# Optimization experiments

Hardware: AMD Instinct MI355X
Metric: run time of the kernel (lower is better)

## Reference

```python
import jax, jax.numpy as jnp
import numpy as np

NUM_HEADS = 8
NUM_POINTS = 4


def _grid_sample_bilinear(img, grid, H, W):
    """torch F.grid_sample(mode='bilinear', padding='zeros', align_corners=False).
    img:  [B, H, W, D]   grid: [B, S, 2] with (x, y) in [-1, 1].
    Returns [B, S, D].
    """
    gx, gy = grid[..., 0], grid[..., 1]
    # align_corners=False pixel mapping
    x = ((gx + 1.0) * W - 1.0) * 0.5
    y = ((gy + 1.0) * H - 1.0) * 0.5
    x0 = jnp.floor(x)
    y0 = jnp.floor(y)
    wx1 = x - x0
    wy1 = y - y0
    x0i = x0.astype(jnp.int32)
    y0i = y0.astype(jnp.int32)
    img_flat = img.reshape(img.shape[0], H * W, img.shape[-1])  # [B, N, D]

    def corner(xi, yi, w):
        valid = (xi >= 0) & (xi < W) & (yi >= 0) & (yi < H)  # zeros padding
        idx = jnp.clip(yi, 0, H - 1) * W + jnp.clip(xi, 0, W - 1)  # [B, S]
        v = jnp.take_along_axis(img_flat, idx[..., None], axis=1)  # [B, S, D]
        return v * (w * valid.astype(img.dtype))[..., None]

    out = corner(x0i, y0i, (1.0 - wx1) * (1.0 - wy1))
    out += corner(x0i + 1, y0i, wx1 * (1.0 - wy1))
    out += corner(x0i, y0i + 1, (1.0 - wx1) * wy1)
    out += corner(x0i + 1, y0i + 1, wx1 * wy1)
    return out


def setup_inputs() -> dict:
    key = jax.random.key(0)
    ks = jax.random.split(key, 12)
    B, Q, D = 4, 1024, 256
    H, W = 128, 128
    nh, npts = NUM_HEADS, NUM_POINTS
    f32 = jnp.float32
    return {
        "query": jax.random.normal(ks[0], (B, Q, D), f32),
        "reference_points": jax.random.uniform(ks[1], (B, Q, 2), f32),
        "value": jax.random.normal(ks[2], (B, H * W, D), f32),
        "W_off": jax.random.normal(ks[3], (D, nh * npts * 2), f32) * 0.02,
        "b_off": jax.random.normal(ks[4], (nh * npts * 2,), f32) * 0.02,
        "W_attn": jax.random.normal(ks[5], (D, nh * npts), f32) * 0.02,
        "b_attn": jax.random.normal(ks[6], (nh * npts,), f32) * 0.02,
        "W_v": jax.random.normal(ks[7], (D, D), f32) * (D ** -0.5),
        "b_v": jnp.zeros((D,), f32),
        "W_out": jax.random.normal(ks[8], (nh * D, D), f32) * ((nh * D) ** -0.5),
        "b_out": jnp.zeros((D,), f32),
        "H": H,
        "W": W,
    }


def reference(query, reference_points, value, W_off, b_off, W_attn, b_attn,
              W_v, b_v, W_out, b_out, H, W):
    B, Q, D = query.shape
    nh, npts = NUM_HEADS, NUM_POINTS
    # learned offsets and per-point attention weights
    offsets = (query @ W_off + b_off).reshape(B, Q, nh, npts, 2)
    attn = jax.nn.softmax((query @ W_attn + b_attn).reshape(B, Q, nh, npts), axis=-1)
    # sampling locations in [-1, 1]
    locs = reference_points[:, :, None, None, :] + offsets * 0.1
    locs = jnp.clip(locs, 0.0, 1.0) * 2.0 - 1.0
    # value projection -> 2D feature map [B, H, W, D]
    img = (value @ W_v + b_v).reshape(B, H, W, D)
    # sample all heads/points at once
    grid = locs.reshape(B, Q * nh * npts, 2)
    sampled = _grid_sample_bilinear(img, grid, H, W).reshape(B, Q, nh, npts, D)
    # weighted reduce over points, concat heads
    weighted = jnp.einsum("bqhpd,bqhp->bqhd", sampled, attn)
    out = weighted.reshape(B, Q, nh * D) @ W_out + b_out
    return out
```

## Files before the change

kernel.cpp:

```cpp
#include <hip/hip_runtime.h>
#include <hip/hip_bf16.h>
#include <math.h>

constexpr int B  = 4;
constexpr int Q  = 1024;
constexpr int D  = 256;
constexpr int NH = 8;
constexpr int NP = 4;
constexpr int H  = 128;
constexpr int W  = 128;
constexpr int HW = H * W;
constexpr int KAUG = 2112;

typedef short   bf16x8  __attribute__((ext_vector_type(8)));
typedef float   f32x4   __attribute__((ext_vector_type(4)));
typedef short   short4v __attribute__((ext_vector_type(4)));
typedef unsigned short ushort8v __attribute__((ext_vector_type(8)));

__device__ inline unsigned short f2bf(float f) {
    union { float f; unsigned u; } v; v.f = f;
    unsigned r = v.u + 0x7fff + ((v.u >> 16) & 1);
    return (unsigned short)(r >> 16);
}
__device__ inline float bf2f(unsigned short s) {
    union { unsigned u; float f; } v; v.u = ((unsigned)s) << 16;
    return v.f;
}

__device__ inline void async16(const void* g, void* l) {
    __builtin_amdgcn_global_load_lds(
        (const __attribute__((address_space(1))) unsigned*)g,
        (__attribute__((address_space(3))) unsigned*)l, 16, 0, 0);
}

__device__ __forceinline__ void gemm64_dbuf(
        unsigned short* __restrict__ lds,
        const unsigned short* __restrict__ A, int lda,
        const unsigned short* __restrict__ Bt, int ldb,
        const float* __restrict__ bias,
        float* __restrict__ C, int ldc, int K, int m0, int n0) {
    const int tid  = threadIdx.x;
    const int lane = tid & 63;
    const int w    = tid >> 6;
    const int wm   = w >> 1, wn = w & 1;

    const int srow = w * 8 + (lane >> 3);
    const int schk = (lane & 7) ^ (lane >> 3);
    const unsigned short* ag0 = A  + (size_t)(m0 + srow)      * lda + schk * 8;
    const unsigned short* ag1 = A  + (size_t)(m0 + srow + 32) * lda + schk * 8;
    const unsigned short* bg0 = Bt + (size_t)(n0 + srow)      * ldb + schk * 8;
    const unsigned short* bg1 = Bt + (size_t)(n0 + srow + 32) * ldb + schk * 8;
    const int l0 = w * 512 + lane * 8;
    const int l1 = l0 + 2048;

    int aoff[2][2], boff[2][2];
    #pragma unroll
    for (int i = 0; i < 2; ++i)
        #pragma unroll
        for (int kk = 0; kk < 2; ++kk) {
            const int ar = wm * 32 + i * 16 + (lane & 15);
            aoff[i][kk] = ar * 64 + ((((lane >> 4) + kk * 4) ^ (ar & 7)) * 8);
            const int br = wn * 32 + i * 16 + (lane & 15);
            boff[i][kk] = br * 64 + ((((lane >> 4) + kk * 4) ^ (br & 7)) * 8);
        }

    f32x4 acc[2][2];
    #pragma unroll
    for (int i = 0; i < 2; ++i)
        #pragma unroll
        for (int j = 0; j < 2; ++j) acc[i][j] = (f32x4){0.f, 0.f, 0.f, 0.f};

    async16(ag0, &lds[0 * 4096 + l0]); async16(ag1, &lds[0 * 4096 + l1]);
    async16(bg0, &lds[1 * 4096 + l0]); async16(bg1, &lds[1 * 4096 + l1]);

    const int niter = K >> 6;
    for (int it = 0; it < niter; ++it) {
        __syncthreads();
        const int cur = (it & 1) * 2;
        if (it + 1 < niter) {
            const int nxt = 2 - cur;
            const int ko  = (it + 1) * 64;
            async16(ag0 + ko, &lds[nxt * 4096 + l0]);
            async16(ag1 + ko, &lds[nxt * 4096 + l1]);
            async16(bg0 + ko, &lds[(nxt + 1) * 4096 + l0]);
            async16(bg1 + ko, &lds[(nxt + 1) * 4096 + l1]);
        }
        bf16x8 af[2][2], bfv[2][2];
        #pragma unroll
        for (int i = 0; i < 2; ++i)
            #pragma unroll
            for (int kk = 0; kk < 2; ++kk) {
                af[i][kk]  = *(const bf16x8*)&lds[cur * 4096 + aoff[i][kk]];
                bfv[i][kk] = *(const bf16x8*)&lds[(cur + 1) * 4096 + boff[i][kk]];
            }
        #pragma unroll
        for (int i = 0; i < 2; ++i)
            #pragma unroll
            for (int j = 0; j < 2; ++j)
                #pragma unroll
                for (int kk = 0; kk < 2; ++kk)
                    acc[i][j] = __builtin_amdgcn_mfma_f32_16x16x32_bf16(
                        af[i][kk], bfv[j][kk], acc[i][j], 0, 0, 0);
    }

    const int colb = n0 + wn * 32 + (lane & 15);
    const int rowb = m0 + wm * 32 + (lane >> 4) * 4;
    #pragma unroll
    for (int j = 0; j < 2; ++j) {
        const int col = colb + j * 16;
        const float bb = bias[col];
        #pragma unroll
        for (int i = 0; i < 2; ++i)
            #pragma unroll
            for (int r = 0; r < 4; ++r)
                C[(size_t)(rowb + i * 16 + r) * ldc + col] = acc[i][j][r] + bb;
    }
}

__device__ __forceinline__ void gemm64_single_t(
        unsigned short* __restrict__ lds,
        const unsigned short* __restrict__ A, int lda,
        const unsigned short* __restrict__ Bt, int ldb,
        unsigned short* __restrict__ Wt, int ldc, int K,
        int m0, int n0, int zblk) {
    const int tid  = threadIdx.x;
    const int lane = tid & 63;
    const int w    = tid >> 6;
    const int wm   = w >> 1, wn = w & 1;
    Bt += (size_t)zblk * 256;

    const int srow = w * 8 + (lane >> 3);
    const int schk = (lane & 7) ^ (lane >> 3);
    const unsigned short* ag0 = A  + (size_t)(m0 + srow)      * lda + schk * 8;
    const unsigned short* ag1 = A  + (size_t)(m0 + srow + 32) * lda + schk * 8;
    const unsigned short* bg0 = Bt + (size_t)(n0 + srow)      * ldb + schk * 8;
    const unsigned short* bg1 = Bt + (size_t)(n0 + srow + 32) * ldb + schk * 8;
    const int l0 = w * 512 + lane * 8;
    const int l1 = l0 + 2048;

    int aoff[2][2], boff[2][2];
    #pragma unroll
    for (int i = 0; i < 2; ++i)
        #pragma unroll
        for (int kk = 0; kk < 2; ++kk) {
            const int ar = wm * 32 + i * 16 + (lane & 15);
            aoff[i][kk] = ar * 64 + ((((lane >> 4) + kk * 4) ^ (ar & 7)) * 8);
            const int br = wn * 32 + i * 16 + (lane & 15);
            boff[i][kk] = br * 64 + ((((lane >> 4) + kk * 4) ^ (br & 7)) * 8);
        }

    f32x4 acc[2][2];
    #pragma unroll
    for (int i = 0; i < 2; ++i)
        #pragma unroll
        for (int j = 0; j < 2; ++j) acc[i][j] = (f32x4){0.f, 0.f, 0.f, 0.f};

    const int niter = K >> 6;
    for (int it = 0; it < niter; ++it) {
        __syncthreads();
        const int ko = it * 64;
        async16(ag0 + ko, &lds[l0]);
        async16(ag1 + ko, &lds[l1]);
        async16(bg0 + ko, &lds[4096 + l0]);
        async16(bg1 + ko, &lds[4096 + l1]);
        __syncthreads();
        bf16x8 af[2][2], bfv[2][2];
        #pragma unroll
        for (int i = 0; i < 2; ++i)
            #pragma unroll
            for (int kk = 0; kk < 2; ++kk) {
                af[i][kk]  = *(const bf16x8*)&lds[aoff[i][kk]];
                bfv[i][kk] = *(const bf16x8*)&lds[4096 + boff[i][kk]];
            }
        #pragma unroll
        for (int i = 0; i < 2; ++i)
            #pragma unroll
            for (int j = 0; j < 2; ++j)
                #pragma unroll
                for (int kk = 0; kk < 2; ++kk)
                    acc[i][j] = __builtin_amdgcn_mfma_f32_16x16x32_bf16(
                        af[i][kk], bfv[j][kk], acc[i][j], 0, 0, 0);
    }

    const int colb = n0 + wn * 32 + (lane & 15);
    const int rowb = m0 + wm * 32 + (lane >> 4) * 4;
    const int ocol = zblk * 256;
    #pragma unroll
    for (int j = 0; j < 2; ++j) {
        const int col = colb + j * 16;
        #pragma unroll
        for (int i = 0; i < 2; ++i)
            #pragma unroll
            for (int r = 0; r < 4; ++r)
                Wt[(size_t)col * ldc + ocol + rowb + i * 16 + r] =
                    f2bf(acc[i][j][r]);
    }
}

constexpr int R1_SG   = 0;
constexpr int R1_BV   = R1_SG   + 128;
constexpr int R1_WV   = R1_BV   + (D * 64) / 256;
constexpr int R1_WOUT = R1_WV   + (D * D) / 1024;
constexpr int R1_CONV = R1_WOUT + (NH * D * D) / 256;
constexpr int R1_END  = R1_CONV + (B * HW * D) / 4096;

__global__ __launch_bounds__(256)
void k_stage1(const float* __restrict__ value,
              const float* __restrict__ query,
              const float* __restrict__ W_off,  const float* __restrict__ b_off,
              const float* __restrict__ W_attn, const float* __restrict__ b_attn,
              const float* __restrict__ b_v,    const float* __restrict__ W_out,
              const float* __restrict__ W_v,
              unsigned short* __restrict__ val_bf,
              float* __restrict__ raw,
              unsigned short* __restrict__ Wout_t,
              unsigned short* __restrict__ Wv_bf,
              unsigned short* __restrict__ WcT) {
    __shared__ __align__(16) float smem[2][16][68];
    const int blk = blockIdx.x;
    const int tid = threadIdx.x;

    if (blk < R1_BV) {
        const int m0 = (blk >> 1) * 64;
        const int n0 = (blk & 1) * 64;
        float (*As)[68] = smem[0];
        float (*Bs)[68] = smem[1];
        const int tx = tid & 15, ty = tid >> 4;
        const int arow = tid >> 2, akg = (tid & 3) * 4;
        const int brow = tid >> 4, bcol = (tid & 15) * 4;

        float acc[4][4] = {};
        for (int k0 = 0; k0 < D; k0 += 16) {
            const float4 av = *(const float4*)&query[(size_t)(m0 + arow) * D + k0 + akg];
            const int kr = k0 + brow;
            const int j  = n0 + bcol;
            float4 bv;
            if (j < 64)      bv = *(const float4*)&W_off[kr * 64 + j];
            else if (j < 96) bv = *(const float4*)&W_attn[kr * 32 + (j - 64)];
            else             bv = (float4){0.f, 0.f, 0.f, 0.f};
            __syncthreads();
            As[akg + 0][arow] = av.x;
            As[akg + 1][arow] = av.y;
            As[akg + 2][arow] = av.z;
            As[akg + 3][arow] = av.w;
            *(float4*)&Bs[brow][bcol] = bv;
            __syncthreads();
            #pragma unroll
            for (int kk = 0; kk < 16; ++kk) {
                const float4 a = *(const float4*)&As[kk][ty * 4];
                const float4 b = *(const float4*)&Bs[kk][tx * 4];
                acc[0][0] += a.x * b.x; acc[0][1] += a.x * b.y; acc[0][2] += a.x * b.z; acc[0][3] += a.x * b.w;
                acc[1][0] += a.y * b.x; acc[1][1] += a.y * b.y; acc[1][2] += a.y * b.z; acc[1][3] += a.y * b.w;
                acc[2][0] += a.z * b.x; acc[2][1] += a.z * b.y; acc[2][2] += a.z * b.z; acc[2][3] += a.z * b.w;
                acc[3][0] += a.w * b.x; acc[3][1] += a.w * b.y; acc[3][2] += a.w * b.z; acc[3][3] += a.w * b.w;
            }
        }
        float bb[4];
        #pragma unroll
        for (int c = 0; c < 4; ++c) {
            const int col = n0 + tx * 4 + c;
            bb[c] = (col < 64) ? b_off[col] : ((col < 96) ? b_attn[col - 64] : 0.0f);
        }
        #pragma unroll
        for (int i = 0; i < 4; ++i) {
            const int m = m0 + ty * 4 + i;
            float4 r;
            r.x = acc[i][0] + bb[0];
            r.y = acc[i][1] + bb[1];
            r.z = acc[i][2] + bb[2];
            r.w = acc[i][3] + bb[3];
            *(float4*)&raw[(size_t)m * 128 + n0 + tx * 4] = r;
        }
    } else if (blk < R1_WV) {
        const int t = (blk - R1_BV) * 256 + tid;
        const int n = t >> 6, c = t & 63;
        float v = 0.0f;
        if (c < 8) {
            #pragma unroll 8
            for (int j = 0; j < D; ++j)
                v += b_v[j] * W_out[((size_t)c * D + j) * D + n];
        }
        WcT[(size_t)n * KAUG + 2048 + c] = f2bf(v);
    } else if (blk < R1_WOUT) {
        const int i = (blk - R1_WV) * 1024 + tid * 4;
        const float4 v = *(const float4*)&W_v[i];
        short4v o;
        o.x = (short)f2bf(v.x); o.y = (short)f2bf(v.y);
        o.z = (short)f2bf(v.z); o.w = (short)f2bf(v.w);
        *(short4v*)&Wv_bf[i] = o;
    } else if (blk < R1_CONV) {
        const int i = (blk - R1_WOUT) * 256 + tid;
        const int n = i >> 11, k = i & 2047;
        Wout_t[i] = f2bf(W_out[(size_t)k * D + n]);
    } else {
        const int base = (blk - R1_CONV) * 4096;
        #pragma unroll
        for (int s = 0; s < 4; ++s) {
            const int i = base + s * 1024 + tid * 4;
            const float4 v = *(const float4*)&value[i];
            short4v o;
            o.x = (short)f2bf(v.x); o.y = (short)f2bf(v.y);
            o.z = (short)f2bf(v.z); o.w = (short)f2bf(v.w);
            *(short4v*)&val_bf[i] = o;
        }
    }
}

constexpr int R2_WC  = B * Q;
constexpr int R2_END = R2_WC + 128;

__global__ __launch_bounds__(256)
void k_stage2(const unsigned short* __restrict__ val,
              const float* __restrict__ raw,
              const float* __restrict__ refpts,
              const unsigned short* __restrict__ Wv_bf,
              const unsigned short* __restrict__ Wout_t,
              unsigned short* __restrict__ sv,
              unsigned short* __restrict__ WcT) {
    __shared__ __align__(16) unsigned short smem[8192];
    const int blk = blockIdx.x;
    const int tid = threadIdx.x;

    if (blk >= R2_WC) {
        const int blkr = blk - R2_WC;
        const int z  = blkr >> 4;
        const int m0 = ((blkr >> 2) & 3) * 64;
        const int n0 = (blkr & 3) * 64;
        gemm64_single_t(smem, Wv_bf, D, Wout_t, NH * D, WcT, KAUG, D,
                        m0, n0, z);
        return;
    }

    const int bq   = blk;
    const int b    = bq >> 10;
    const int lane = tid & 63;
    const int w    = tid >> 6;

    float* s_raw = (float*)smem;
    int*   s_off = (int*)((char*)smem + 512);
    float* s_wgt = (float*)((char*)smem + 1024);

    if (tid < 128) s_raw[tid] = raw[(size_t)bq * 128 + tid];
    __syncthreads();

    if (tid < NH * NP) {
        const int h = tid >> 2;
        float m = -1e30f;
        #pragma unroll
        for (int p = 0; p < NP; ++p) m = fmaxf(m, s_raw[64 + h * 4 + p]);
        float s = 0.0f;
        #pragma unroll
        for (int p = 0; p < NP; ++p) s += __expf(s_raw[64 + h * 4 + p] - m);
        const float a = __expf(s_raw[64 + tid] - m) / s;

        const float refx = refpts[(size_t)bq * 2 + 0];
        const float refy = refpts[(size_t)bq * 2 + 1];
        const float gx = fminf(fmaxf(refx + s_raw[tid * 2 + 0] * 0.1f, 0.0f), 1.0f) * 2.0f - 1.0f;
        const float gy = fminf(fmaxf(refy + s_raw[tid * 2 + 1] * 0.1f, 0.0f), 1.0f) * 2.0f - 1.0f;
        const float x  = ((gx + 1.0f) * (float)W - 1.0f) * 0.5f;
        const float y  = ((gy + 1.0f) * (float)H - 1.0f) * 0.5f;
        const float x0f = floorf(x), y0f = floorf(y);
        const float wx1 = x - x0f,  wy1 = y - y0f;
        const float wx0 = 1.0f - wx1, wy0 = 1.0f - wy1;
        const int x0 = (int)x0f, y0 = (int)y0f;
        const int x1 = x0 + 1,  y1 = y0 + 1;
        const float vx0 = (x0 >= 0 && x0 < W) ? 1.0f : 0.0f;
        const float vx1 = (x1 >= 0 && x1 < W) ? 1.0f : 0.0f;
        const float vy0 = (y0 >= 0 && y0 < H) ? 1.0f : 0.0f;
        const float vy1 = (y1 >= 0 && y1 < H) ? 1.0f : 0.0f;
        const int xc0 = min(max(x0, 0), W - 1);
        const int xc1 = min(max(x1, 0), W - 1);
        const int yc0 = min(max(y0, 0), H - 1);
        const int yc1 = min(max(y1, 0), H - 1);
        s_off[tid * 4 + 0] = yc0 * W + xc0;
        s_off[tid * 4 + 1] = yc0 * W + xc1;
        s_off[tid * 4 + 2] = yc1 * W + xc0;
        s_off[tid * 4 + 3] = yc1 * W + xc1;
        s_wgt[tid * 4 + 0] = a * wx0 * wy0 * vx0 * vy0;
        s_wgt[tid * 4 + 1] = a * wx1 * wy0 * vx1 * vy0;
        s_wgt[tid * 4 + 2] = a * wx0 * wy1 * vx0 * vy1;
        s_wgt[tid * 4 + 3] = a * wx1 * wy1 * vx1 * vy1;
    }
    __syncthreads();

    if (tid < 8) {
        float S = 0.0f;
        #pragma unroll
        for (int c = 0; c < 16; ++c) S += s_wgt[tid * 16 + c];
        sv[(size_t)bq * KAUG + 2048 + tid] = f2bf(S);
    } else if (tid < 64) {
        sv[(size_t)bq * KAUG + 2048 + tid] = 0;
    }

    const int half = lane >> 5;
    const int l5   = lane & 31;
    const unsigned short* ib = val + (size_t)b * HW * D + l5 * 8;

    ushort8v vb[16];
    float    wg[16];
    #pragma unroll
    for (int j = 0; j < 16; ++j) {
        const int flat = w * 32 + j * 2 + half;
        wg[j] = s_wgt[flat];
        vb[j] = *(const ushort8v*)(ib + (size_t)s_off[flat] * D);
    }

    float acc[2][8] = {};
    #pragma unroll
    for (int j = 0; j < 16; ++j) {
        const int g = j >> 3;
        #pragma unroll
        for (int k = 0; k < 8; ++k)
            acc[g][k] += wg[j] * bf2f(vb[j][k]);
    }

    #pragma unroll
    for (int hh = 0; hh < 2; ++hh) {
        float comb[8];
        #pragma unroll
        for (int k = 0; k < 8; ++k)
            comb[k] = acc[hh][k] + __shfl_xor(acc[hh][k], 32, 64);
        if (half == 0) {
            const int h = w * 2 + hh;
            ushort8v o;
            #pragma unroll
            for (int k = 0; k < 8; ++k) o[k] = f2bf(comb[k]);
            *(ushort8v*)&sv[(size_t)bq * KAUG + h * D + l5 * 8] = o;
        }
    }
}

__global__ __launch_bounds__(256)
void k_stage3(const unsigned short* __restrict__ sv,
              const unsigned short* __restrict__ WcT,
              const float* __restrict__ b_out,
              float* __restrict__ out) {
    __shared__ __align__(16) unsigned short smem[16384];
    gemm64_dbuf(smem, sv, KAUG, WcT, KAUG, b_out, out, D, KAUG,
                blockIdx.x * 64, blockIdx.y * 64);
}

extern "C" void kernel_launch(void* const* d_in, const int* in_sizes, int n_in,
                              void* d_out, int out_size, void* d_ws, size_t ws_size,
                              hipStream_t stream) {
    const float* query  = (const float*)d_in[0];
    const float* refpts = (const float*)d_in[1];
    const float* value  = (const float*)d_in[2];
    const float* W_off  = (const float*)d_in[3];
    const float* b_off  = (const float*)d_in[4];
    const float* W_attn = (const float*)d_in[5];
    const float* b_attn = (const float*)d_in[6];
    const float* W_v    = (const float*)d_in[7];
    const float* b_v    = (const float*)d_in[8];
    const float* W_out  = (const float*)d_in[9];
    const float* b_out  = (const float*)d_in[10];
    float* out = (float*)d_out;

    char* wsb = (char*)d_ws;
    unsigned short* val_bf  = (unsigned short*)(wsb);
    unsigned short* sv      = (unsigned short*)(wsb + 33554432);
    unsigned short* WcT     = (unsigned short*)(wsb + 50855936);
    unsigned short* Wout_t  = (unsigned short*)(wsb + 51937280);
    unsigned short* Wv_bf   = (unsigned short*)(wsb + 52985856);
    float*          raw     = (float*)(wsb + 53116928);

    k_stage1<<<R1_END, 256, 0, stream>>>(value, query, W_off, b_off,
                                         W_attn, b_attn, b_v, W_out, W_v,
                                         val_bf, raw, Wout_t, Wv_bf, WcT);

    k_stage2<<<R2_END, 256, 0, stream>>>(val_bf, raw, refpts, Wv_bf, Wout_t,
                                         sv, WcT);

    {
        dim3 grid((B * Q) / 64, D / 64);
        k_stage3<<<grid, 256, 0, stream>>>(sv, WcT, b_out, out);
    }
}
```

Measured before the change: 175.1 us.

## Fuse weight conversion into combined-weight GEMM and retile output GEMM

The combined weight WcT = W_v·W_out GEMM moves from stage2 into stage1, and it now converts fp32 W_v and W_out to bf16 on the fly into LDS. This drops the separate Wv_bf/Wout_t conversion passes and their workspace round trips. Stage2 becomes a pure sampling kernel with static shared memory. Stage3 switches to 32x64 tiles, giving twice as many blocks for better CU occupancy, at the cost of less reuse of the B operand per block.

```diff
diff --git a/kernel.cpp b/kernel.cpp
--- a/kernel.cpp
+++ b/kernel.cpp
@@ -33,175 +33,10 @@
         (__attribute__((address_space(3))) unsigned*)l, 16, 0, 0);
 }
 
-__device__ __forceinline__ void gemm64_dbuf(
-        unsigned short* __restrict__ lds,
-        const unsigned short* __restrict__ A, int lda,
-        const unsigned short* __restrict__ Bt, int ldb,
-        const float* __restrict__ bias,
-        float* __restrict__ C, int ldc, int K, int m0, int n0) {
-    const int tid  = threadIdx.x;
-    const int lane = tid & 63;
-    const int w    = tid >> 6;
-    const int wm   = w >> 1, wn = w & 1;
-
-    const int srow = w * 8 + (lane >> 3);
-    const int schk = (lane & 7) ^ (lane >> 3);
-    const unsigned short* ag0 = A  + (size_t)(m0 + srow)      * lda + schk * 8;
-    const unsigned short* ag1 = A  + (size_t)(m0 + srow + 32) * lda + schk * 8;
-    const unsigned short* bg0 = Bt + (size_t)(n0 + srow)      * ldb + schk * 8;
-    const unsigned short* bg1 = Bt + (size_t)(n0 + srow + 32) * ldb + schk * 8;
-    const int l0 = w * 512 + lane * 8;
-    const int l1 = l0 + 2048;
-
-    int aoff[2][2], boff[2][2];
-    #pragma unroll
-    for (int i = 0; i < 2; ++i)
-        #pragma unroll
-        for (int kk = 0; kk < 2; ++kk) {
-            const int ar = wm * 32 + i * 16 + (lane & 15);
-            aoff[i][kk] = ar * 64 + ((((lane >> 4) + kk * 4) ^ (ar & 7)) * 8);
-            const int br = wn * 32 + i * 16 + (lane & 15);
-            boff[i][kk] = br * 64 + ((((lane >> 4) + kk * 4) ^ (br & 7)) * 8);
-        }
-
-    f32x4 acc[2][2];
-    #pragma unroll
-    for (int i = 0; i < 2; ++i)
-        #pragma unroll
-        for (int j = 0; j < 2; ++j) acc[i][j] = (f32x4){0.f, 0.f, 0.f, 0.f};
-
-    async16(ag0, &lds[0 * 4096 + l0]); async16(ag1, &lds[0 * 4096 + l1]);
-    async16(bg0, &lds[1 * 4096 + l0]); async16(bg1, &lds[1 * 4096 + l1]);
-
-    const int niter = K >> 6;
-    for (int it = 0; it < niter; ++it) {
-        __syncthreads();
-        const int cur = (it & 1) * 2;
-        if (it + 1 < niter) {
-            const int nxt = 2 - cur;
-            const int ko  = (it + 1) * 64;
-            async16(ag0 + ko, &lds[nxt * 4096 + l0]);
-            async16(ag1 + ko, &lds[nxt * 4096 + l1]);
-            async16(bg0 + ko, &lds[(nxt + 1) * 4096 + l0]);
-            async16(bg1 + ko, &lds[(nxt + 1) * 4096 + l1]);
-        }
-        bf16x8 af[2][2], bfv[2][2];
-        #pragma unroll
-        for (int i = 0; i < 2; ++i)
-            #pragma unroll
-            for (int kk = 0; kk < 2; ++kk) {
-                af[i][kk]  = *(const bf16x8*)&lds[cur * 4096 + aoff[i][kk]];
-                bfv[i][kk] = *(const bf16x8*)&lds[(cur + 1) * 4096 + boff[i][kk]];
-            }
-        #pragma unroll
-        for (int i = 0; i < 2; ++i)
-            #pragma unroll
-            for (int j = 0; j < 2; ++j)
-                #pragma unroll
-                for (int kk = 0; kk < 2; ++kk)
-                    acc[i][j] = __builtin_amdgcn_mfma_f32_16x16x32_bf16(
-                        af[i][kk], bfv[j][kk], acc[i][j], 0, 0, 0);
-    }
-
-    const int colb = n0 + wn * 32 + (lane & 15);
-    const int rowb = m0 + wm * 32 + (lane >> 4) * 4;
-    #pragma unroll
-    for (int j = 0; j < 2; ++j) {
-        const int col = colb + j * 16;
-        const float bb = bias[col];
-        #pragma unroll
-        for (int i = 0; i < 2; ++i)
-            #pragma unroll
-            for (int r = 0; r < 4; ++r)
-                C[(size_t)(rowb + i * 16 + r) * ldc + col] = acc[i][j][r] + bb;
-    }
-}
-
-__device__ __forceinline__ void gemm64_single_t(
-        unsigned short* __restrict__ lds,
-        const unsigned short* __restrict__ A, int lda,
-        const unsigned short* __restrict__ Bt, int ldb,
-        unsigned short* __restrict__ Wt, int ldc, int K,
-        int m0, int n0, int zblk) {
-    const int tid  = threadIdx.x;
-    const int lane = tid & 63;
-    const int w    = tid >> 6;
-    const int wm   = w >> 1, wn = w & 1;
-    Bt += (size_t)zblk * 256;
-
-    const int srow = w * 8 + (lane >> 3);
-    const int schk = (lane & 7) ^ (lane >> 3);
-    const unsigned short* ag0 = A  + (size_t)(m0 + srow)      * lda + schk * 8;
-    const unsigned short* ag1 = A  + (size_t)(m0 + srow + 32) * lda + schk * 8;
-    const unsigned short* bg0 = Bt + (size_t)(n0 + srow)      * ldb + schk * 8;
-    const unsigned short* bg1 = Bt + (size_t)(n0 + srow + 32) * ldb + schk * 8;
-    const int l0 = w * 512 + lane * 8;
-    const int l1 = l0 + 2048;
-
-    int aoff[2][2], boff[2][2];
-    #pragma unroll
-    for (int i = 0; i < 2; ++i)
-        #pragma unroll
-        for (int kk = 0; kk < 2; ++kk) {
-            const int ar = wm * 32 + i * 16 + (lane & 15);
-            aoff[i][kk] = ar * 64 + ((((lane >> 4) + kk * 4) ^ (ar & 7)) * 8);
-            const int br = wn * 32 + i * 16 + (lane & 15);
-            boff[i][kk] = br * 64 + ((((lane >> 4) + kk * 4) ^ (br & 7)) * 8);
-        }
-
-    f32x4 acc[2][2];
-    #pragma unroll
-    for (int i = 0; i < 2; ++i)
-        #pragma unroll
-        for (int j = 0; j < 2; ++j) acc[i][j] = (f32x4){0.f, 0.f, 0.f, 0.f};
-
-    const int niter = K >> 6;
-    for (int it = 0; it < niter; ++it) {
-        __syncthreads();
-        const int ko = it * 64;
-        async16(ag0 + ko, &lds[l0]);
-        async16(ag1 + ko, &lds[l1]);
-        async16(bg0 + ko, &lds[4096 + l0]);
-        async16(bg1 + ko, &lds[4096 + l1]);
-        __syncthreads();
-        bf16x8 af[2][2], bfv[2][2];
-        #pragma unroll
-        for (int i = 0; i < 2; ++i)
-            #pragma unroll
-            for (int kk = 0; kk < 2; ++kk) {
-                af[i][kk]  = *(const bf16x8*)&lds[aoff[i][kk]];
-                bfv[i][kk] = *(const bf16x8*)&lds[4096 + boff[i][kk]];
-            }
-        #pragma unroll
-        for (int i = 0; i < 2; ++i)
-            #pragma unroll
-            for (int j = 0; j < 2; ++j)
-                #pragma unroll
-                for (int kk = 0; kk < 2; ++kk)
-                    acc[i][j] = __builtin_amdgcn_mfma_f32_16x16x32_bf16(
-                        af[i][kk], bfv[j][kk], acc[i][j], 0, 0, 0);
-    }
-
-    const int colb = n0 + wn * 32 + (lane & 15);
-    const int rowb = m0 + wm * 32 + (lane >> 4) * 4;
-    const int ocol = zblk * 256;
-    #pragma unroll
-    for (int j = 0; j < 2; ++j) {
-        const int col = colb + j * 16;
-        #pragma unroll
-        for (int i = 0; i < 2; ++i)
-            #pragma unroll
-            for (int r = 0; r < 4; ++r)
-                Wt[(size_t)col * ldc + ocol + rowb + i * 16 + r] =
-                    f2bf(acc[i][j][r]);
-    }
-}
-
 constexpr int R1_SG   = 0;
-constexpr int R1_BV   = R1_SG   + 128;
-constexpr int R1_WV   = R1_BV   + (D * 64) / 256;
-constexpr int R1_WOUT = R1_WV   + (D * D) / 1024;
-constexpr int R1_CONV = R1_WOUT + (NH * D * D) / 256;
+constexpr int R1_WC   = R1_SG + 128;
+constexpr int R1_BV   = R1_WC + 128;
+constexpr int R1_CONV = R1_BV + (D * 64) / 256;
 constexpr int R1_END  = R1_CONV + (B * HW * D) / 4096;
 
 __global__ __launch_bounds__(256)
@@ -213,18 +48,16 @@
               const float* __restrict__ W_v,
               unsigned short* __restrict__ val_bf,
               float* __restrict__ raw,
-              unsigned short* __restrict__ Wout_t,
-              unsigned short* __restrict__ Wv_bf,
               unsigned short* __restrict__ WcT) {
-    __shared__ __align__(16) float smem[2][16][68];
+    __shared__ __align__(16) unsigned char smemraw[16384];
     const int blk = blockIdx.x;
     const int tid = threadIdx.x;
 
-    if (blk < R1_BV) {
+    if (blk < R1_WC) {
         const int m0 = (blk >> 1) * 64;
         const int n0 = (blk & 1) * 64;
-        float (*As)[68] = smem[0];
-        float (*Bs)[68] = smem[1];
+        float (*As)[68] = (float (*)[68])smemraw;
+        float (*Bs)[68] = As + 16;
         const int tx = tid & 15, ty = tid >> 4;
         const int arow = tid >> 2, akg = (tid & 3) * 4;
         const int brow = tid >> 4, bcol = (tid & 15) * 4;
@@ -271,7 +104,96 @@
             r.w = acc[i][3] + bb[3];
             *(float4*)&raw[(size_t)m * 128 + n0 + tx * 4] = r;
         }
-    } else if (blk < R1_WV) {
+    } else if (blk < R1_BV) {
+        const int blkr = blk - R1_WC;
+        const int z  = blkr >> 4;
+        const int m0 = ((blkr >> 2) & 3) * 64;
+        const int n0 = (blkr & 3) * 64;
+        unsigned short* As = (unsigned short*)smemraw;
+        unsigned short* Bs = As + 4096;
+        const int lane = tid & 63;
+        const int w    = tid >> 6;
+        const int wm   = w >> 1, wn = w & 1;
+
+        int aoff[2][2], boff[2][2];
+        #pragma unroll
+        for (int i = 0; i < 2; ++i)
+            #pragma unroll
+            for (int kk = 0; kk < 2; ++kk) {
+                const int ar = wm * 32 + i * 16 + (lane & 15);
+                aoff[i][kk] = ar * 64 + ((((lane >> 4) + kk * 4) ^ (ar & 7)) * 8);
+                const int br = wn * 32 + i * 16 + (lane & 15);
+                boff[i][kk] = br * 64 + ((((lane >> 4) + kk * 4) ^ (br & 7)) * 8);
+            }
+
+        f32x4 acc[2][2];
+        #pragma unroll
+        for (int i = 0; i < 2; ++i)
+            #pragma unroll
+            for (int j = 0; j < 2; ++j) acc[i][j] = (f32x4){0.f, 0.f, 0.f, 0.f};
+
+        for (int it = 0; it < 4; ++it) {
+            const int k0 = it * 64;
+            __syncthreads();
+            #pragma unroll
+            for (int s = 0; s < 2; ++s) {
+                const int cc = tid + s * 256;
+                const int r = cc >> 3, c = cc & 7;
+                const float4 v0 = *(const float4*)&W_v[(size_t)(m0 + r) * D + k0 + c * 8];
+                const float4 v1 = *(const float4*)&W_v[(size_t)(m0 + r) * D + k0 + c * 8 + 4];
+                ushort8v o;
+                o[0] = f2bf(v0.x); o[1] = f2bf(v0.y); o[2] = f2bf(v0.z); o[3] = f2bf(v0.w);
+                o[4] = f2bf(v1.x); o[5] = f2bf(v1.y); o[6] = f2bf(v1.z); o[7] = f2bf(v1.w);
+                *(ushort8v*)&As[r * 64 + ((c ^ (r & 7)) * 8)] = o;
+            }
+            {
+                const int n = tid & 63, kseg = tid >> 6;
+                float vj[16];
+                #pragma unroll
+                for (int j = 0; j < 16; ++j)
+                    vj[j] = W_out[(size_t)(z * 256 + k0 + kseg * 16 + j) * D + n0 + n];
+                #pragma unroll
+                for (int jj = 0; jj < 2; ++jj) {
+                    ushort8v o;
+                    #pragma unroll
+                    for (int q = 0; q < 8; ++q) o[q] = f2bf(vj[jj * 8 + q]);
+                    const int c = kseg * 2 + jj;
+                    *(ushort8v*)&Bs[n * 64 + ((c ^ (n & 7)) * 8)] = o;
+                }
+            }
+            __syncthreads();
+            bf16x8 af[2][2], bfv[2][2];
+            #pragma unroll
+            for (int i = 0; i < 2; ++i)
+                #pragma unroll
+                for (int kk = 0; kk < 2; ++kk) {
+                    af[i][kk]  = *(const bf16x8*)&As[aoff[i][kk]];
+                    bfv[i][kk] = *(const bf16x8*)&Bs[boff[i][kk]];
+                }
+            #pragma unroll
+            for (int i = 0; i < 2; ++i)
+                #pragma unroll
+                for (int j = 0; j < 2; ++j)
+                    #pragma unroll
+                    for (int kk = 0; kk < 2; ++kk)
+                        acc[i][j] = __builtin_amdgcn_mfma_f32_16x16x32_bf16(
+                            af[i][kk], bfv[j][kk], acc[i][j], 0, 0, 0);
+        }
+
+        const int colb = n0 + wn * 32 + (lane & 15);
+        const int rowb = m0 + wm * 32 + (lane >> 4) * 4;
+        const int ocol = z * 256;
+        #pragma unroll
+        for (int j = 0; j < 2; ++j) {
+            const int col = colb + j * 16;
+            #pragma unroll
+            for (int i = 0; i < 2; ++i)
+                #pragma unroll
+                for (int r = 0; r < 4; ++r)
+                    WcT[(size_t)col * KAUG + ocol + rowb + i * 16 + r] =
+                        f2bf(acc[i][j][r]);
+        }
+    } else if (blk < R1_CONV) {
         const int t = (blk - R1_BV) * 256 + tid;
         const int n = t >> 6, c = t & 63;
         float v = 0.0f;
@@ -281,17 +203,6 @@
                 v += b_v[j] * W_out[((size_t)c * D + j) * D + n];
         }
         WcT[(size_t)n * KAUG + 2048 + c] = f2bf(v);
-    } else if (blk < R1_WOUT) {
-        const int i = (blk - R1_WV) * 1024 + tid * 4;
-        const float4 v = *(const float4*)&W_v[i];
-        short4v o;
-        o.x = (short)f2bf(v.x); o.y = (short)f2bf(v.y);
-        o.z = (short)f2bf(v.z); o.w = (short)f2bf(v.w);
-        *(short4v*)&Wv_bf[i] = o;
-    } else if (blk < R1_CONV) {
-        const int i = (blk - R1_WOUT) * 256 + tid;
-        const int n = i >> 11, k = i & 2047;
-        Wout_t[i] = f2bf(W_out[(size_t)k * D + n]);
     } else {
         const int base = (blk - R1_CONV) * 4096;
         #pragma unroll
@@ -306,39 +217,20 @@
     }
 }
 
-constexpr int R2_WC  = B * Q;
-constexpr int R2_END = R2_WC + 128;
-
 __global__ __launch_bounds__(256)
 void k_stage2(const unsigned short* __restrict__ val,
               const float* __restrict__ raw,
               const float* __restrict__ refpts,
-              const unsigned short* __restrict__ Wv_bf,
-              const unsigned short* __restrict__ Wout_t,
-              unsigned short* __restrict__ sv,
-              unsigned short* __restrict__ WcT) {
-    __shared__ __align__(16) unsigned short smem[8192];
-    const int blk = blockIdx.x;
-    const int tid = threadIdx.x;
-
-    if (blk >= R2_WC) {
-        const int blkr = blk - R2_WC;
-        const int z  = blkr >> 4;
-        const int m0 = ((blkr >> 2) & 3) * 64;
-        const int n0 = (blkr & 3) * 64;
-        gemm64_single_t(smem, Wv_bf, D, Wout_t, NH * D, WcT, KAUG, D,
-                        m0, n0, z);
-        return;
-    }
-
-    const int bq   = blk;
+              unsigned short* __restrict__ sv) {
+    const int bq   = blockIdx.x;
     const int b    = bq >> 10;
+    const int tid  = threadIdx.x;
     const int lane = tid & 63;
     const int w    = tid >> 6;
 
-    float* s_raw = (float*)smem;
-    int*   s_off = (int*)((char*)smem + 512);
-    float* s_wgt = (float*)((char*)smem + 1024);
+    __shared__ float s_raw[128];
+    __shared__ int   s_off[128];
+    __shared__ float s_wgt[128];
 
     if (tid < 128) s_raw[tid] = raw[(size_t)bq * 128 + tid];
     __syncthreads();
@@ -435,9 +327,78 @@
               const unsigned short* __restrict__ WcT,
               const float* __restrict__ b_out,
               float* __restrict__ out) {
-    __shared__ __align__(16) unsigned short smem[16384];
-    gemm64_dbuf(smem, sv, KAUG, WcT, KAUG, b_out, out, D, KAUG,
-                blockIdx.x * 64, blockIdx.y * 64);
+    __shared__ __align__(16) unsigned short lds[12288];
+
+    const int tid  = threadIdx.x;
+    const int lane = tid & 63;
+    const int w    = tid >> 6;
+    const int m0 = blockIdx.x * 32, n0 = blockIdx.y * 64;
+
+    const int srow = w * 8 + (lane >> 3);
+    const int schk = (lane & 7) ^ (lane >> 3);
+    const unsigned short* ag  = sv  + (size_t)(m0 + srow)      * KAUG + schk * 8;
+    const unsigned short* bg0 = WcT + (size_t)(n0 + srow)      * KAUG + schk * 8;
+    const unsigned short* bg1 = WcT + (size_t)(n0 + srow + 32) * KAUG + schk * 8;
+    const int la = w * 512 + lane * 8;
+    const int lb = la;
+
+    int aoff[2][2], boff[2];
+    #pragma unroll
+    for (int i = 0; i < 2; ++i)
+        #pragma unroll
+        for (int kk = 0; kk < 2; ++kk) {
+            const int ar = i * 16 + (lane & 15);
+            aoff[i][kk] = ar * 64 + ((((lane >> 4) + kk * 4) ^ (ar & 7)) * 8);
+        }
+    #pragma unroll
+    for (int kk = 0; kk < 2; ++kk) {
+        const int br = w * 16 + (lane & 15);
+        boff[kk] = br * 64 + ((((lane >> 4) + kk * 4) ^ (br & 7)) * 8);
+    }
+
+    f32x4 acc[2];
+    acc[0] = (f32x4){0.f, 0.f, 0.f, 0.f};
+    acc[1] = (f32x4){0.f, 0.f, 0.f, 0.f};
+
+    async16(ag,  &lds[0 + la]);
+    async16(bg0, &lds[2048 + lb]);
+    async16(bg1, &lds[2048 + 2048 + lb]);
+
+    const int niter = KAUG >> 6;
+    for (int it = 0; it < niter; ++it) {
+        __syncthreads();
+        const int cur = (it & 1) * 6144;
+        if (it + 1 < niter) {
+            const int nxt = 6144 - cur;
+            const int ko  = (it + 1) * 64;
+            async16(ag + ko,  &lds[nxt + la]);
+            async16(bg0 + ko, &lds[nxt + 2048 + lb]);
+            async16(bg1 + ko, &lds[nxt + 4096 + lb]);
+        }
+        bf16x8 af[2][2], bfv[2];
+        #pragma unroll
+        for (int kk = 0; kk < 2; ++kk) {
+            bfv[kk] = *(const bf16x8*)&lds[cur + 2048 + boff[kk]];
+            #pragma unroll
+            for (int i = 0; i < 2; ++i)
+                af[i][kk] = *(const bf16x8*)&lds[cur + aoff[i][kk]];
+        }
+        #pragma unroll
+        for (int i = 0; i < 2; ++i)
+            #pragma unroll
+            for (int kk = 0; kk < 2; ++kk)
+                acc[i] = __builtin_amdgcn_mfma_f32_16x16x32_bf16(
+                    af[i][kk], bfv[kk], acc[i], 0, 0, 0);
+    }
+
+    const int col = n0 + w * 16 + (lane & 15);
+    const float bb = b_out[col];
+    const int rowb = m0 + (lane >> 4) * 4;
+    #pragma unroll
+    for (int i = 0; i < 2; ++i)
+        #pragma unroll
+        for (int r = 0; r < 4; ++r)
+            out[(size_t)(rowb + i * 16 + r) * D + col] = acc[i][r] + bb;
 }
 
 extern "C" void kernel_launch(void* const* d_in, const int* in_sizes, int n_in,
@@ -457,22 +418,19 @@
     float* out = (float*)d_out;
 
     char* wsb = (char*)d_ws;
-    unsigned short* val_bf  = (unsigned short*)(wsb);
-    unsigned short* sv      = (unsigned short*)(wsb + 33554432);
-    unsigned short* WcT     = (unsigned short*)(wsb + 50855936);
-    unsigned short* Wout_t  = (unsigned short*)(wsb + 51937280);
-    unsigned short* Wv_bf   = (unsigned short*)(wsb + 52985856);
-    float*          raw     = (float*)(wsb + 53116928);
+    unsigned short* val_bf = (unsigned short*)(wsb);
+    unsigned short* sv     = (unsigned short*)(wsb + 33554432);
+    unsigned short* WcT    = (unsigned short*)(wsb + 50855936);
+    float*          raw    = (float*)(wsb + 51937280);
 
     k_stage1<<<R1_END, 256, 0, stream>>>(value, query, W_off, b_off,
                                          W_attn, b_attn, b_v, W_out, W_v,
-                                         val_bf, raw, Wout_t, Wv_bf, WcT);
-
-    k_stage2<<<R2_END, 256, 0, stream>>>(val_bf, raw, refpts, Wv_bf, Wout_t,
-                                         sv, WcT);
+                                         val_bf, raw, WcT);
+
+    k_stage2<<<B * Q, 256, 0, stream>>>(val_bf, raw, refpts, sv);
 
     {
-        dim3 grid((B * Q) / 64, D / 64);
+        dim3 grid((B * Q) / 32, D / 64);
         k_stage3<<<grid, 256, 0, stream>>>(sv, WcT, b_out, out);
     }
 }
```

After: 170.1 us. 1.03x faster.
